# Performance work log

Hardware: AMD Instinct MI355X
Metric: run time of the kernel (lower is better)

The kernel has to match this reference:

```python
import jax, jax.numpy as jnp
import numpy as np

EPS = 1e-7  # keras.backend.epsilon()


def setup_inputs() -> dict:
    key = jax.random.key(0)
    kx, kw, ku = jax.random.split(key, 3)
    B, S, F = 16, 4096, 512
    x = jax.random.normal(kx, (B, S, F), dtype=jnp.float32)
    # glorot-uniform-scaled weights
    limW = np.sqrt(6.0 / (F + F)).astype(np.float32)
    W = jax.random.uniform(kw, (F, F), dtype=jnp.float32, minval=-limW, maxval=limW)
    b = jnp.zeros((F,), dtype=jnp.float32)
    limu = np.sqrt(6.0 / (F + 1)).astype(np.float32)
    u = jax.random.uniform(ku, (F,), dtype=jnp.float32, minval=-limu, maxval=limu)
    return {"x": x, "W": W, "b": b, "u": u}


def reference(x, W, b, u):
    # x: [B,S,F]  W: [F,F]  b: [F]  u: [F]
    h = jnp.tanh(jnp.einsum('bsf,fg->bsg', x, W) + b)   # [B,S,F]
    scores = jnp.einsum('bsf,f->bs', h, u)              # [B,S]
    e = jnp.exp(scores)
    # NOTE: faithful to the source, normalization is GLOBAL over all B*S scores
    a = e / (jnp.sum(e) + EPS)                          # [B,S]
    out = jnp.einsum('bsf,bs->bf', x, a)                # [B,F] weighted-sum pool over steps
    return out
```

## Files before the change

kernel.cpp:

```cpp
#include <hip/hip_runtime.h>
#include <stdint.h>

#define EPSV 1e-7f
#define FDIM 512
#define BK 64
#define NROWS 65536

typedef __bf16 bf16_t;
typedef bf16_t bf16x8 __attribute__((ext_vector_type(8)));
typedef unsigned short ushort8 __attribute__((ext_vector_type(8)));
typedef float f32x4 __attribute__((ext_vector_type(4)));

#define AS1 __attribute__((address_space(1)))
#define AS3 __attribute__((address_space(3)))

__device__ __forceinline__ unsigned short f2bf(float f) {
  union { float f; unsigned int u; } c; c.f = f;
  unsigned int u = c.u;
  unsigned int r = u + 0x7fffu + ((u >> 16) & 1u);
  return (unsigned short)(r >> 16);
}
__device__ __forceinline__ float bf2f(unsigned short s) {
  union { unsigned int u; float f; } c; c.u = ((unsigned int)s) << 16;
  return c.f;
}

__device__ __forceinline__ float fast_tanh(float x) {
  x = fminf(15.0f, fmaxf(-15.0f, x));
  float t = __expf(2.0f * x);
  return 1.0f - 2.0f * __builtin_amdgcn_rcpf(t + 1.0f);
}

__global__ void convert_W(const float* __restrict__ W, unsigned short* __restrict__ Wt) {
  __shared__ unsigned short tile[32][34];
  const int t = threadIdx.x;
  const int tx = t & 31, ty = t >> 5;
  const int bn = blockIdx.x & 15, bk = blockIdx.x >> 4;
  const int k0 = bk * 32, n0 = bn * 32;
#pragma unroll
  for (int i = 0; i < 4; ++i) {
    int r = ty + i * 8;
    tile[r][tx] = f2bf(W[(size_t)(k0 + r) * FDIM + n0 + tx]);
  }
  __syncthreads();
#pragma unroll
  for (int i = 0; i < 4; ++i) {
    int r = ty + i * 8;
    Wt[(size_t)(n0 + r) * FDIM + k0 + tx] = tile[tx][r];
  }
}

__global__ __launch_bounds__(256) void convert_x(const float* __restrict__ x,
                                                 unsigned short* __restrict__ xbf) {
  size_t i = ((size_t)blockIdx.x * 256 + threadIdx.x) * 8;
  float4 lo = *(const float4*)(x + i);
  float4 hi = *(const float4*)(x + i + 4);
  ushort8 v;
  v[0] = f2bf(lo.x); v[1] = f2bf(lo.y); v[2] = f2bf(lo.z); v[3] = f2bf(lo.w);
  v[4] = f2bf(hi.x); v[5] = f2bf(hi.y); v[6] = f2bf(hi.z); v[7] = f2bf(hi.w);
  *(ushort8*)(xbf + i) = v;
}

template <bool ABF>
__global__ __launch_bounds__(256, 4) void gemm_score(
    const float* __restrict__ x, const unsigned short* __restrict__ xbf,
    const unsigned short* __restrict__ Wt,
    const float* __restrict__ bvec, const float* __restrict__ uvec,
    float* __restrict__ spart) {
  __shared__ unsigned short sA[128 * BK];
  __shared__ unsigned short sB[128 * BK];
  __shared__ float score_s[128];
  __shared__ float ub_s[128], bb_s[128];

  const int t = threadIdx.x;
  const int lane = t & 63;
  const int w = t >> 6;
  const int wm = w & 1;
  const int wn = w >> 1;
  const int quad = lane >> 4;
  const int l15 = lane & 15;
  const int nch = blockIdx.x >> 9;
  const int rt = blockIdx.x & 511;
  const int m0 = rt * 128;
  const int col0 = nch * 128;

  if (t < 128) {
    score_s[t] = 0.0f;
    ub_s[t] = uvec[col0 + t];
    bb_s[t] = bvec[col0 + t];
  }

  f32x4 acc[4][4];
#pragma unroll
  for (int mi = 0; mi < 4; ++mi)
#pragma unroll
    for (int ni = 0; ni < 4; ++ni) acc[mi][ni] = (f32x4){0.f, 0.f, 0.f, 0.f};

  for (int kc = 0; kc < FDIM / BK; ++kc) {
    const int kbase = kc * BK;
    if constexpr (ABF) {
#pragma unroll
      for (int i = 0; i < 4; ++i) {
        int rb = w * 32 + i * 8;
        int rl = rb + (lane >> 3);
        int j = (lane & 7) ^ (rl & 7);
        const unsigned short* g =
            xbf + (size_t)(m0 + rl) * FDIM + kbase + j * 8;
        unsigned short* l = (unsigned short*)(sA + rb * 64);
        __builtin_amdgcn_global_load_lds((AS1 void*)(g), (AS3 void*)(l), 16, 0, 0);
      }
    } else {
#pragma unroll
      for (int p = 0; p < 4; ++p) {
        int slot = t + 256 * p;
        int row = slot >> 3;
        int j = (slot & 7) ^ (row & 7);
        const float* g = x + (size_t)(m0 + row) * FDIM + kbase + j * 8;
        float4 lo = *(const float4*)g;
        float4 hi = *(const float4*)(g + 4);
        ushort8 v;
        v[0] = f2bf(lo.x); v[1] = f2bf(lo.y); v[2] = f2bf(lo.z); v[3] = f2bf(lo.w);
        v[4] = f2bf(hi.x); v[5] = f2bf(hi.y); v[6] = f2bf(hi.z); v[7] = f2bf(hi.w);
        *(ushort8*)(void*)(sA + slot * 8) = v;
      }
    }
#pragma unroll
    for (int i = 0; i < 4; ++i) {
      int nb = w * 32 + i * 8;
      int nl = nb + (lane >> 3);
      int j = (lane & 7) ^ (nl & 7);
      const unsigned short* g =
          Wt + (size_t)(col0 + nl) * FDIM + kbase + j * 8;
      unsigned short* l = (unsigned short*)(sB + nb * 64);
      __builtin_amdgcn_global_load_lds((AS1 void*)(g), (AS3 void*)(l), 16, 0, 0);
    }
    __syncthreads();
#pragma unroll
    for (int ks = 0; ks < 2; ++ks) {
      bf16x8 af[4], bfr[4];
#pragma unroll
      for (int mi = 0; mi < 4; ++mi) {
        int row = wm * 64 + mi * 16 + l15;
        int phys = (ks * 4 + quad) ^ (row & 7);
        af[mi] = *(const bf16x8*)(const void*)(sA + row * 64 + phys * 8);
      }
#pragma unroll
      for (int ni = 0; ni < 4; ++ni) {
        int row = wn * 64 + ni * 16 + l15;
        int phys = (ks * 4 + quad) ^ (row & 7);
        bfr[ni] = *(const bf16x8*)(const void*)(sB + row * 64 + phys * 8);
      }
#pragma unroll
      for (int mi = 0; mi < 4; ++mi)
#pragma unroll
        for (int ni = 0; ni < 4; ++ni)
          acc[mi][ni] = __builtin_amdgcn_mfma_f32_16x16x32_bf16(
              af[mi], bfr[ni], acc[mi][ni], 0, 0, 0);
    }
    __syncthreads();
  }

  float sc[4][4];
#pragma unroll
  for (int mi = 0; mi < 4; ++mi)
#pragma unroll
    for (int r = 0; r < 4; ++r) sc[mi][r] = 0.0f;
#pragma unroll
  for (int ni = 0; ni < 4; ++ni) {
    int cl = wn * 64 + ni * 16 + l15;
    float uu = ub_s[cl], bb = bb_s[cl];
#pragma unroll
    for (int mi = 0; mi < 4; ++mi)
#pragma unroll
      for (int r = 0; r < 4; ++r)
        sc[mi][r] += uu * fast_tanh(acc[mi][ni][r] + bb);
  }
#pragma unroll
  for (int mi = 0; mi < 4; ++mi)
#pragma unroll
    for (int r = 0; r < 4; ++r) {
      float v = sc[mi][r];
      v += __shfl_xor(v, 1); v += __shfl_xor(v, 2);
      v += __shfl_xor(v, 4); v += __shfl_xor(v, 8);
      if (l15 == 0)
        atomicAdd(&score_s[wm * 64 + mi * 16 + quad * 4 + r], v);
    }
  __syncthreads();
  if (t < 128) spart[(size_t)nch * NROWS + m0 + t] = score_s[t];
}

__global__ void score_exp(float* __restrict__ spart, float* __restrict__ sumE) {
  __shared__ float ws_[4];
  const int t = threadIdx.x;
  const int i = blockIdx.x * 256 + t;
  float s = spart[i] + spart[i + NROWS] + spart[i + 2 * NROWS] + spart[i + 3 * NROWS];
  float e = __expf(s);
  spart[i] = e;
  float v = e;
  v += __shfl_xor(v, 1);  v += __shfl_xor(v, 2);  v += __shfl_xor(v, 4);
  v += __shfl_xor(v, 8);  v += __shfl_xor(v, 16); v += __shfl_xor(v, 32);
  if ((t & 63) == 0) ws_[t >> 6] = v;
  __syncthreads();
  if (t == 0) atomicAdd(sumE, ws_[0] + ws_[1] + ws_[2] + ws_[3]);
}

__global__ __launch_bounds__(256, 8) void pool_part(
    const unsigned short* __restrict__ xbf, const float* __restrict__ e,
    float* __restrict__ ppool) {
  __shared__ float e_s[32];
  __shared__ float red[4][FDIM];
  const int t = threadIdx.x;
  const int c8 = t & 63, rg = t >> 6;
  const int r0 = blockIdx.x * 32;
  if (t < 32) e_s[t] = e[r0 + t];
  __syncthreads();
  float a[8];
#pragma unroll
  for (int j = 0; j < 8; ++j) a[j] = 0.0f;
  for (int it = 0; it < 8; ++it) {
    int row = rg * 8 + it;
    ushort8 v = *(const ushort8*)(xbf + (size_t)(r0 + row) * FDIM + c8 * 8);
    float wg = e_s[row];
#pragma unroll
    for (int j = 0; j < 8; ++j) a[j] += bf2f(v[j]) * wg;
  }
  *(float4*)&red[rg][c8 * 8]     = (float4){a[0], a[1], a[2], a[3]};
  *(float4*)&red[rg][c8 * 8 + 4] = (float4){a[4], a[5], a[6], a[7]};
  __syncthreads();
  int c = t, c2 = t + 256;
  float s0 = red[0][c] + red[1][c] + red[2][c] + red[3][c];
  float s1 = red[0][c2] + red[1][c2] + red[2][c2] + red[3][c2];
  ppool[(size_t)blockIdx.x * FDIM + c]  = s0;
  ppool[(size_t)blockIdx.x * FDIM + c2] = s1;
}

__global__ __launch_bounds__(256) void pool_reduce(
    const float* __restrict__ ppool, const float* __restrict__ sumE,
    float* __restrict__ out) {
  const int i = blockIdx.x * 256 + threadIdx.x;
  const int b = i >> 9, f = i & 511;
  float s = 0.0f;
  const float* p = ppool + (size_t)b * 128 * FDIM + f;
  for (int c = 0; c < 128; ++c) s += p[(size_t)c * FDIM];
  out[i] = s / (*sumE + EPSV);
}

__global__ __launch_bounds__(256) void pool_k(
    const float* __restrict__ x, const float* __restrict__ e,
    const float* __restrict__ sumE, float* __restrict__ out) {
  __shared__ float e_s[128];
  __shared__ float4 red[128];
  const int t = threadIdx.x;
  const int b = blockIdx.x >> 5, chunk = blockIdx.x & 31;
  const int g0 = b * 4096 + chunk * 128;
  if (t < 128) e_s[t] = e[g0 + t];
  __syncthreads();
  const int parity = t >> 7, f4 = t & 127;
  float ax = 0.f, ay = 0.f, az = 0.f, aw = 0.f;
  for (int r = 0; r < 64; ++r) {
    int row = r * 2 + parity;
    const float4 xv = *(const float4*)(x + (size_t)(g0 + row) * FDIM + f4 * 4);
    float wgt = e_s[row];
    ax += xv.x * wgt; ay += xv.y * wgt; az += xv.z * wgt; aw += xv.w * wgt;
  }
  if (parity) red[f4] = (float4){ax, ay, az, aw};
  __syncthreads();
  if (!parity) {
    float4 o = red[f4];
    float inv = 1.0f / (*sumE + EPSV);
    float* op = out + (size_t)b * FDIM + f4 * 4;
    atomicAdd(op + 0, (ax + o.x) * inv);
    atomicAdd(op + 1, (ay + o.y) * inv);
    atomicAdd(op + 2, (az + o.z) * inv);
    atomicAdd(op + 3, (aw + o.w) * inv);
  }
}

extern "C" void kernel_launch(void* const* d_in, const int* in_sizes, int n_in,
                              void* d_out, int out_size, void* d_ws, size_t ws_size,
                              hipStream_t stream) {
  (void)in_sizes; (void)n_in;
  const float* x = (const float*)d_in[0];
  const float* W = (const float*)d_in[1];
  const float* b = (const float*)d_in[2];
  const float* u = (const float*)d_in[3];
  float* out = (float*)d_out;

  char* p = (char*)d_ws;
  unsigned short* Wt = (unsigned short*)p;            p += (size_t)FDIM * FDIM * 2;
  float* spart = (float*)p;                           p += (size_t)4 * NROWS * 4;
  float* sumE = (float*)p;                            p += 256;
  float* ppool = (float*)p;                           p += (size_t)2048 * FDIM * 4;
  unsigned short* xbf = (unsigned short*)p;           p += (size_t)NROWS * FDIM * 2;
  const size_t need = (size_t)(p - (char*)d_ws);
  const bool big = ws_size >= need;

  hipMemsetAsync(sumE, 0, sizeof(float), stream);
  convert_W<<<dim3(256), dim3(256), 0, stream>>>(W, Wt);

  if (big) {
    convert_x<<<dim3(NROWS * FDIM / (256 * 8)), dim3(256), 0, stream>>>(x, xbf);
    gemm_score<true><<<dim3(2048), dim3(256), 0, stream>>>(x, xbf, Wt, b, u, spart);
    score_exp<<<dim3(NROWS / 256), dim3(256), 0, stream>>>(spart, sumE);
    pool_part<<<dim3(2048), dim3(256), 0, stream>>>(xbf, spart, ppool);
    pool_reduce<<<dim3(32), dim3(256), 0, stream>>>(ppool, sumE, out);
  } else {
    hipMemsetAsync(d_out, 0, (size_t)out_size * sizeof(float), stream);
    gemm_score<false><<<dim3(2048), dim3(256), 0, stream>>>(x, xbf, Wt, b, u, spart);
    score_exp<<<dim3(NROWS / 256), dim3(256), 0, stream>>>(spart, sumE);
    pool_k<<<dim3(512), dim3(256), 0, stream>>>(x, spart, sumE, out);
  }
}
```

Measured before the change: 275.4 us.

## Fuse GEMM, score, exp and pooling into one kernel with LDS-resident x tile

Replaces the separate x-conversion, GEMM-score, exp and pooling kernels with one fused kernel per 128-row block. The block converts its full 128x512 slice of x to bf16 in LDS once, loops over all 512 output columns while streaming W tiles, then computes exp and the weighted pool directly from the LDS copy. This removes the bf16 x round trip through global memory, the partial-score buffer and several launches. In exchange it needs 128KB+ of LDS per block (low occupancy, 512 threads) and uses a single-buffered W pipeline with two barriers per k-step.

New measurement: 258.2 us. -6.2%, faster.

```diff
diff --git a/kernel.cpp b/kernel.cpp
--- a/kernel.cpp
+++ b/kernel.cpp
@@ -3,6 +3,7 @@
 
 #define EPSV 1e-7f
 #define FDIM 512
+#define ROWS 128
 #define BK 64
 #define NROWS 65536
 
@@ -50,27 +51,28 @@
   }
 }
 
-__global__ __launch_bounds__(256) void convert_x(const float* __restrict__ x,
-                                                 unsigned short* __restrict__ xbf) {
-  size_t i = ((size_t)blockIdx.x * 256 + threadIdx.x) * 8;
-  float4 lo = *(const float4*)(x + i);
-  float4 hi = *(const float4*)(x + i + 4);
-  ushort8 v;
-  v[0] = f2bf(lo.x); v[1] = f2bf(lo.y); v[2] = f2bf(lo.z); v[3] = f2bf(lo.w);
-  v[4] = f2bf(hi.x); v[5] = f2bf(hi.y); v[6] = f2bf(hi.z); v[7] = f2bf(hi.w);
-  *(ushort8*)(xbf + i) = v;
-}
-
-template <bool ABF>
-__global__ __launch_bounds__(256, 4) void gemm_score(
-    const float* __restrict__ x, const unsigned short* __restrict__ xbf,
-    const unsigned short* __restrict__ Wt,
+#define ISSUE_B(col0_, kb_)                                                    \
+  do {                                                                         \
+    _Pragma("unroll") for (int i_ = 0; i_ < 2; ++i_) {                         \
+      const int rb_ = w * 16 + i_ * 8;                                         \
+      const int rl_ = rb_ + (lane >> 3);                                       \
+      const int j_ = (lane & 7) ^ (rl_ & 7);                                   \
+      const unsigned short* g_ =                                               \
+          Wt + (size_t)((col0_) + rl_) * FDIM + (kb_) + j_ * 8;                \
+      unsigned short* l_ = (unsigned short*)(sB + rb_ * BK);                   \
+      __builtin_amdgcn_global_load_lds((AS1 void*)(g_), (AS3 void*)(l_), 16,   \
+                                       0, 0);                                  \
+    }                                                                          \
+  } while (0)
+
+__global__ __launch_bounds__(512, 2) void fused_score_pool(
+    const float* __restrict__ x, const unsigned short* __restrict__ Wt,
     const float* __restrict__ bvec, const float* __restrict__ uvec,
-    float* __restrict__ spart) {
-  __shared__ unsigned short sA[128 * BK];
-  __shared__ unsigned short sB[128 * BK];
-  __shared__ float score_s[128];
-  __shared__ float ub_s[128], bb_s[128];
+    float* __restrict__ ppool, float* __restrict__ sumE) {
+  __shared__ alignas(16) unsigned short sA[ROWS * FDIM];
+  __shared__ alignas(16) unsigned short sB[128 * BK];
+  __shared__ float score_s[ROWS];
+  __shared__ float e_s[ROWS];
 
   const int t = threadIdx.x;
   const int lane = t & 63;
@@ -79,102 +81,86 @@
   const int wn = w >> 1;
   const int quad = lane >> 4;
   const int l15 = lane & 15;
-  const int nch = blockIdx.x >> 9;
-  const int rt = blockIdx.x & 511;
-  const int m0 = rt * 128;
-  const int col0 = nch * 128;
-
-  if (t < 128) {
-    score_s[t] = 0.0f;
-    ub_s[t] = uvec[col0 + t];
-    bb_s[t] = bvec[col0 + t];
-  }
-
-  f32x4 acc[4][4];
+  const int m0 = blockIdx.x * ROWS;
+
+  if (t < ROWS) score_s[t] = 0.0f;
+
+  ISSUE_B(0, 0);
+
+#pragma unroll
+  for (int p = 0; p < 16; ++p) {
+    const int row = p * 8 + w;
+    const float* g = x + (size_t)(m0 + row) * FDIM + lane * 8;
+    float4 lo = *(const float4*)g;
+    float4 hi = *(const float4*)(g + 4);
+    ushort8 v;
+    v[0] = f2bf(lo.x); v[1] = f2bf(lo.y); v[2] = f2bf(lo.z); v[3] = f2bf(lo.w);
+    v[4] = f2bf(hi.x); v[5] = f2bf(hi.y); v[6] = f2bf(hi.z); v[7] = f2bf(hi.w);
+    const int jp = lane ^ (row & 7);
+    *(ushort8*)(void*)(sA + row * FDIM + jp * 8) = v;
+  }
+  __syncthreads();
+
+  float sc[4][4];
 #pragma unroll
   for (int mi = 0; mi < 4; ++mi)
 #pragma unroll
-    for (int ni = 0; ni < 4; ++ni) acc[mi][ni] = (f32x4){0.f, 0.f, 0.f, 0.f};
-
-  for (int kc = 0; kc < FDIM / BK; ++kc) {
-    const int kbase = kc * BK;
-    if constexpr (ABF) {
-#pragma unroll
-      for (int i = 0; i < 4; ++i) {
-        int rb = w * 32 + i * 8;
-        int rl = rb + (lane >> 3);
-        int j = (lane & 7) ^ (rl & 7);
-        const unsigned short* g =
-            xbf + (size_t)(m0 + rl) * FDIM + kbase + j * 8;
-        unsigned short* l = (unsigned short*)(sA + rb * 64);
-        __builtin_amdgcn_global_load_lds((AS1 void*)(g), (AS3 void*)(l), 16, 0, 0);
+    for (int r = 0; r < 4; ++r) sc[mi][r] = 0.0f;
+
+  for (int nc = 0; nc < 4; ++nc) {
+    const int col0 = nc * 128;
+    f32x4 acc[4][2];
+#pragma unroll
+    for (int mi = 0; mi < 4; ++mi)
+#pragma unroll
+      for (int ni = 0; ni < 2; ++ni) acc[mi][ni] = (f32x4){0.f, 0.f, 0.f, 0.f};
+
+    for (int kc = 0; kc < 8; ++kc) {
+      bf16x8 bfr[2][2];
+#pragma unroll
+      for (int ni = 0; ni < 2; ++ni)
+#pragma unroll
+        for (int ks = 0; ks < 2; ++ks) {
+          const int nrow = wn * 32 + ni * 16 + l15;
+          const int phys = (ks * 4 + quad) ^ (nrow & 7);
+          bfr[ni][ks] = *(const bf16x8*)(const void*)(sB + nrow * BK + phys * 8);
+        }
+      __syncthreads();
+
+      const int s = nc * 8 + kc + 1;
+      if (s < 32) ISSUE_B((s >> 3) * 128, (s & 7) * BK);
+
+#pragma unroll
+      for (int ks = 0; ks < 2; ++ks) {
+        bf16x8 af[4];
+#pragma unroll
+        for (int mi = 0; mi < 4; ++mi) {
+          const int row = wm * 64 + mi * 16 + l15;
+          const int phys = kc * 8 + ((ks * 4 + quad) ^ (row & 7));
+          af[mi] = *(const bf16x8*)(const void*)(sA + row * FDIM + phys * 8);
+        }
+#pragma unroll
+        for (int mi = 0; mi < 4; ++mi)
+#pragma unroll
+          for (int ni = 0; ni < 2; ++ni)
+            acc[mi][ni] = __builtin_amdgcn_mfma_f32_16x16x32_bf16(
+                af[mi], bfr[ni][ks], acc[mi][ni], 0, 0, 0);
       }
-    } else {
-#pragma unroll
-      for (int p = 0; p < 4; ++p) {
-        int slot = t + 256 * p;
-        int row = slot >> 3;
-        int j = (slot & 7) ^ (row & 7);
-        const float* g = x + (size_t)(m0 + row) * FDIM + kbase + j * 8;
-        float4 lo = *(const float4*)g;
-        float4 hi = *(const float4*)(g + 4);
-        ushort8 v;
-        v[0] = f2bf(lo.x); v[1] = f2bf(lo.y); v[2] = f2bf(lo.z); v[3] = f2bf(lo.w);
-        v[4] = f2bf(hi.x); v[5] = f2bf(hi.y); v[6] = f2bf(hi.z); v[7] = f2bf(hi.w);
-        *(ushort8*)(void*)(sA + slot * 8) = v;
-      }
+      __syncthreads();
     }
-#pragma unroll
-    for (int i = 0; i < 4; ++i) {
-      int nb = w * 32 + i * 8;
-      int nl = nb + (lane >> 3);
-      int j = (lane & 7) ^ (nl & 7);
-      const unsigned short* g =
-          Wt + (size_t)(col0 + nl) * FDIM + kbase + j * 8;
-      unsigned short* l = (unsigned short*)(sB + nb * 64);
-      __builtin_amdgcn_global_load_lds((AS1 void*)(g), (AS3 void*)(l), 16, 0, 0);
+
+#pragma unroll
+    for (int ni = 0; ni < 2; ++ni) {
+      const int cl = col0 + wn * 32 + ni * 16 + l15;
+      const float uu = uvec[cl], bb = bvec[cl];
+#pragma unroll
+      for (int mi = 0; mi < 4; ++mi)
+#pragma unroll
+        for (int r = 0; r < 4; ++r)
+          sc[mi][r] += uu * fast_tanh(acc[mi][ni][r] + bb);
     }
-    __syncthreads();
-#pragma unroll
-    for (int ks = 0; ks < 2; ++ks) {
-      bf16x8 af[4], bfr[4];
-#pragma unroll
-      for (int mi = 0; mi < 4; ++mi) {
-        int row = wm * 64 + mi * 16 + l15;
-        int phys = (ks * 4 + quad) ^ (row & 7);
-        af[mi] = *(const bf16x8*)(const void*)(sA + row * 64 + phys * 8);
-      }
-#pragma unroll
-      for (int ni = 0; ni < 4; ++ni) {
-        int row = wn * 64 + ni * 16 + l15;
-        int phys = (ks * 4 + quad) ^ (row & 7);
-        bfr[ni] = *(const bf16x8*)(const void*)(sB + row * 64 + phys * 8);
-      }
-#pragma unroll
-      for (int mi = 0; mi < 4; ++mi)
-#pragma unroll
-        for (int ni = 0; ni < 4; ++ni)
-          acc[mi][ni] = __builtin_amdgcn_mfma_f32_16x16x32_bf16(
-              af[mi], bfr[ni], acc[mi][ni], 0, 0, 0);
-    }
-    __syncthreads();
-  }
-
-  float sc[4][4];
-#pragma unroll
-  for (int mi = 0; mi < 4; ++mi)
-#pragma unroll
-    for (int r = 0; r < 4; ++r) sc[mi][r] = 0.0f;
-#pragma unroll
-  for (int ni = 0; ni < 4; ++ni) {
-    int cl = wn * 64 + ni * 16 + l15;
-    float uu = ub_s[cl], bb = bb_s[cl];
-#pragma unroll
-    for (int mi = 0; mi < 4; ++mi)
-#pragma unroll
-      for (int r = 0; r < 4; ++r)
-        sc[mi][r] += uu * fast_tanh(acc[mi][ni][r] + bb);
-  }
+  }
+
 #pragma unroll
   for (int mi = 0; mi < 4; ++mi)
 #pragma unroll
@@ -186,100 +172,57 @@
         atomicAdd(&score_s[wm * 64 + mi * 16 + quad * 4 + r], v);
     }
   __syncthreads();
-  if (t < 128) spart[(size_t)nch * NROWS + m0 + t] = score_s[t];
-}
-
-__global__ void score_exp(float* __restrict__ spart, float* __restrict__ sumE) {
-  __shared__ float ws_[4];
-  const int t = threadIdx.x;
-  const int i = blockIdx.x * 256 + t;
-  float s = spart[i] + spart[i + NROWS] + spart[i + 2 * NROWS] + spart[i + 3 * NROWS];
-  float e = __expf(s);
-  spart[i] = e;
-  float v = e;
-  v += __shfl_xor(v, 1);  v += __shfl_xor(v, 2);  v += __shfl_xor(v, 4);
-  v += __shfl_xor(v, 8);  v += __shfl_xor(v, 16); v += __shfl_xor(v, 32);
-  if ((t & 63) == 0) ws_[t >> 6] = v;
-  __syncthreads();
-  if (t == 0) atomicAdd(sumE, ws_[0] + ws_[1] + ws_[2] + ws_[3]);
-}
-
-__global__ __launch_bounds__(256, 8) void pool_part(
-    const unsigned short* __restrict__ xbf, const float* __restrict__ e,
-    float* __restrict__ ppool) {
-  __shared__ float e_s[32];
-  __shared__ float red[4][FDIM];
-  const int t = threadIdx.x;
-  const int c8 = t & 63, rg = t >> 6;
-  const int r0 = blockIdx.x * 32;
-  if (t < 32) e_s[t] = e[r0 + t];
-  __syncthreads();
+
+  if (t < ROWS) {
+    const float e = __expf(score_s[t]);
+    e_s[t] = e;
+    float v = e;
+    v += __shfl_xor(v, 1);  v += __shfl_xor(v, 2);  v += __shfl_xor(v, 4);
+    v += __shfl_xor(v, 8);  v += __shfl_xor(v, 16); v += __shfl_xor(v, 32);
+    if (lane == 0) atomicAdd(sumE, v);
+  }
+  __syncthreads();
+
   float a[8];
 #pragma unroll
-  for (int j = 0; j < 8; ++j) a[j] = 0.0f;
-  for (int it = 0; it < 8; ++it) {
-    int row = rg * 8 + it;
-    ushort8 v = *(const ushort8*)(xbf + (size_t)(r0 + row) * FDIM + c8 * 8);
-    float wg = e_s[row];
-#pragma unroll
-    for (int j = 0; j < 8; ++j) a[j] += bf2f(v[j]) * wg;
-  }
-  *(float4*)&red[rg][c8 * 8]     = (float4){a[0], a[1], a[2], a[3]};
-  *(float4*)&red[rg][c8 * 8 + 4] = (float4){a[4], a[5], a[6], a[7]};
-  __syncthreads();
-  int c = t, c2 = t + 256;
-  float s0 = red[0][c] + red[1][c] + red[2][c] + red[3][c];
-  float s1 = red[0][c2] + red[1][c2] + red[2][c2] + red[3][c2];
-  ppool[(size_t)blockIdx.x * FDIM + c]  = s0;
-  ppool[(size_t)blockIdx.x * FDIM + c2] = s1;
-}
-
-__global__ __launch_bounds__(256) void pool_reduce(
+  for (int jj = 0; jj < 8; ++jj) a[jj] = 0.0f;
+#pragma unroll
+  for (int rr = 0; rr < 16; ++rr) {
+    const int row = w * 16 + rr;
+    const int jp = lane ^ (row & 7);
+    const ushort8 v = *(const ushort8*)(const void*)(sA + row * FDIM + jp * 8);
+    const float wg = e_s[row];
+#pragma unroll
+    for (int jj = 0; jj < 8; ++jj) a[jj] += bf2f(v[jj]) * wg;
+  }
+  float* red = (float*)sB;
+  *(float4*)&red[w * FDIM + lane * 8]     = (float4){a[0], a[1], a[2], a[3]};
+  *(float4*)&red[w * FDIM + lane * 8 + 4] = (float4){a[4], a[5], a[6], a[7]};
+  __syncthreads();
+  {
+    float sv = 0.0f;
+#pragma unroll
+    for (int g = 0; g < 8; ++g) sv += red[g * FDIM + t];
+    ppool[(size_t)blockIdx.x * FDIM + t] = sv;
+  }
+}
+
+__global__ __launch_bounds__(256) void finalize(
     const float* __restrict__ ppool, const float* __restrict__ sumE,
     float* __restrict__ out) {
   const int i = blockIdx.x * 256 + threadIdx.x;
   const int b = i >> 9, f = i & 511;
+  const float* p = ppool + (size_t)b * 32 * FDIM + f;
   float s = 0.0f;
-  const float* p = ppool + (size_t)b * 128 * FDIM + f;
-  for (int c = 0; c < 128; ++c) s += p[(size_t)c * FDIM];
+#pragma unroll
+  for (int c = 0; c < 32; ++c) s += p[(size_t)c * FDIM];
   out[i] = s / (*sumE + EPSV);
-}
-
-__global__ __launch_bounds__(256) void pool_k(
-    const float* __restrict__ x, const float* __restrict__ e,
-    const float* __restrict__ sumE, float* __restrict__ out) {
-  __shared__ float e_s[128];
-  __shared__ float4 red[128];
-  const int t = threadIdx.x;
-  const int b = blockIdx.x >> 5, chunk = blockIdx.x & 31;
-  const int g0 = b * 4096 + chunk * 128;
-  if (t < 128) e_s[t] = e[g0 + t];
-  __syncthreads();
-  const int parity = t >> 7, f4 = t & 127;
-  float ax = 0.f, ay = 0.f, az = 0.f, aw = 0.f;
-  for (int r = 0; r < 64; ++r) {
-    int row = r * 2 + parity;
-    const float4 xv = *(const float4*)(x + (size_t)(g0 + row) * FDIM + f4 * 4);
-    float wgt = e_s[row];
-    ax += xv.x * wgt; ay += xv.y * wgt; az += xv.z * wgt; aw += xv.w * wgt;
-  }
-  if (parity) red[f4] = (float4){ax, ay, az, aw};
-  __syncthreads();
-  if (!parity) {
-    float4 o = red[f4];
-    float inv = 1.0f / (*sumE + EPSV);
-    float* op = out + (size_t)b * FDIM + f4 * 4;
-    atomicAdd(op + 0, (ax + o.x) * inv);
-    atomicAdd(op + 1, (ay + o.y) * inv);
-    atomicAdd(op + 2, (az + o.z) * inv);
-    atomicAdd(op + 3, (aw + o.w) * inv);
-  }
 }
 
 extern "C" void kernel_launch(void* const* d_in, const int* in_sizes, int n_in,
                               void* d_out, int out_size, void* d_ws, size_t ws_size,
                               hipStream_t stream) {
-  (void)in_sizes; (void)n_in;
+  (void)in_sizes; (void)n_in; (void)out_size; (void)ws_size;
   const float* x = (const float*)d_in[0];
   const float* W = (const float*)d_in[1];
   const float* b = (const float*)d_in[2];
@@ -287,27 +230,13 @@
   float* out = (float*)d_out;
 
   char* p = (char*)d_ws;
-  unsigned short* Wt = (unsigned short*)p;            p += (size_t)FDIM * FDIM * 2;
-  float* spart = (float*)p;                           p += (size_t)4 * NROWS * 4;
-  float* sumE = (float*)p;                            p += 256;
-  float* ppool = (float*)p;                           p += (size_t)2048 * FDIM * 4;
-  unsigned short* xbf = (unsigned short*)p;           p += (size_t)NROWS * FDIM * 2;
-  const size_t need = (size_t)(p - (char*)d_ws);
-  const bool big = ws_size >= need;
+  unsigned short* Wt = (unsigned short*)p;  p += (size_t)FDIM * FDIM * 2;
+  float* sumE = (float*)p;                  p += 256;
+  float* ppool = (float*)p;                 p += (size_t)(NROWS / ROWS) * FDIM * 4;
 
   hipMemsetAsync(sumE, 0, sizeof(float), stream);
   convert_W<<<dim3(256), dim3(256), 0, stream>>>(W, Wt);
-
-  if (big) {
-    convert_x<<<dim3(NROWS * FDIM / (256 * 8)), dim3(256), 0, stream>>>(x, xbf);
-    gemm_score<true><<<dim3(2048), dim3(256), 0, stream>>>(x, xbf, Wt, b, u, spart);
-    score_exp<<<dim3(NROWS / 256), dim3(256), 0, stream>>>(spart, sumE);
-    pool_part<<<dim3(2048), dim3(256), 0, stream>>>(xbf, spart, ppool);
-    pool_reduce<<<dim3(32), dim3(256), 0, stream>>>(ppool, sumE, out);
-  } else {
-    hipMemsetAsync(d_out, 0, (size_t)out_size * sizeof(float), stream);
-    gemm_score<false><<<dim3(2048), dim3(256), 0, stream>>>(x, xbf, Wt, b, u, spart);
-    score_exp<<<dim3(NROWS / 256), dim3(256), 0, stream>>>(spart, sumE);
-    pool_k<<<dim3(512), dim3(256), 0, stream>>>(x, spart, sumE, out);
-  }
-}
+  fused_score_pool<<<dim3(NROWS / ROWS), dim3(512), 0, stream>>>(
+      x, Wt, b, u, ppool, sumE);
+  finalize<<<dim3(32), dim3(256), 0, stream>>>(ppool, sumE, out);
+}
```
